# Kernel tuning notes

Measured on AMD Instinct MI355X. Metric: run time of the kernel, lower is better.

Reference implementation:

```python
import jax, jax.numpy as jnp
import numpy as np

T, S = 24, 200
N = T * S            # 4800 product-graph nodes
C_IN, C_W, C_OUT = 8, 32, 1
K = 3                # polynomial filter order
NB = 2               # number of GTCNN blocks


def setup_inputs() -> dict:
    key = jax.random.key(0)
    ks = jax.random.split(key, 12)
    At = jax.random.uniform(ks[0], (T, T), dtype=jnp.float32)
    At = (At + At.T) * 0.5  # symmetric, positive degrees
    As = jax.random.uniform(ks[1], (S, S), dtype=jnp.float32)
    As = (As + As.T) * 0.5
    return {
        "x_in": jax.random.normal(ks[2], (N, C_IN), dtype=jnp.float32),
        "Adj_t": At,
        "Adj_s": As,
        "H": jax.random.normal(ks[3], (NB, K, C_W, C_W), dtype=jnp.float32) * 0.1,
        "s": jax.random.normal(ks[4], (NB, 4), dtype=jnp.float32),
        "W_first": jax.random.normal(ks[5], (C_IN, C_W), dtype=jnp.float32) * 0.1,
        "b_first": jnp.zeros((C_W,), jnp.float32),
        "W_last": jax.random.normal(ks[6], (C_W, C_OUT), dtype=jnp.float32) * 0.1,
        "b_last": jnp.zeros((C_OUT,), jnp.float32),
        "mlp_W1": jax.random.normal(ks[7], (NB, C_IN + C_W, C_W), dtype=jnp.float32) * 0.1,
        "mlp_b1": jnp.zeros((NB, C_W), jnp.float32),
        "mlp_W2": jax.random.normal(ks[8], (NB, C_W, C_W), dtype=jnp.float32) * 0.1,
        "mlp_b2": jnp.zeros((NB, C_W), jnp.float32),
    }


def _sym_norm(A):
    # D^{-1/2} A D^{-1/2} / 2 as in GTCNN_v2.__init__
    dinv = 1.0 / jnp.sqrt(jnp.sum(A, axis=1))
    return (A * dinv[:, None] * dinv[None, :]) * 0.5


def reference(x_in, Adj_t, Adj_s, H, s, W_first, b_first, W_last, b_last,
              mlp_W1, mlp_b1, mlp_W2, mlp_b2):
    At = _sym_norm(Adj_t)
    As = _sym_norm(Adj_s)
    I_t = jnp.eye(T, dtype=At.dtype)
    I_s = jnp.eye(S, dtype=As.dtype)
    I_N = jnp.eye(N, dtype=At.dtype)

    x = x_in @ W_first + b_first  # [N, C_W]
    for b in range(NB):
        sb = s[b]
        # product-graph adjacency: s0*I + s1*(I_t (x) As) + s2*(At (x) I_s) + s3*(At (x) As)
        Adj = (sb[0] * I_N
               + sb[1] * jnp.kron(I_t, As)
               + sb[2] * jnp.kron(At, I_s)
               + sb[3] * jnp.kron(At, As))
        # sum_k A^k x H_k via the recurrence p_{k} = A p_{k-1} (same math as matrix_power)
        p = x
        acc = p @ H[b, 0]
        for k in range(1, K):
            p = Adj @ p
            acc = acc + p @ H[b, k]
        xt = jnp.tanh(acc)
        feat = jnp.concatenate([xt, x_in], axis=-1)  # [N, C_W + C_in]
        h = jax.nn.relu(feat @ mlp_W1[b] + mlp_b1[b])
        x = h @ mlp_W2[b] + mlp_b2[b]
    return x @ W_last + b_last  # [N, C_out]
```

## Files before the change

### kernel.cpp

```cpp
#include <hip/hip_runtime.h>
#include <math.h>

#define TT 24
#define SS 200
#define CIN 8
#define CW 32
#define NSC 6400
#define NTOT 153600

#define DSOFF   0
#define ATOFF   256
#define AT2OFF  832
#define XOFF    1408
#define M0AOFF  155008
#define M0BOFF  308608
#define M1OFF   462208
#define M2OFF   615808
#define M3OFF   769408

template<bool FIRST>
__global__ __launch_bounds__(1024)
void kSp(const float* __restrict__ xin, const float* __restrict__ At,
         const float* __restrict__ As, const float* __restrict__ Wf,
         const float* __restrict__ bf, const float* __restrict__ svec,
         float* __restrict__ ws, int b)
{
    __shared__ float4 sXd[SS];
    __shared__ float4 sX[SS];
    __shared__ float4 sU[SS];
    __shared__ float4 spart[4][SS];
    __shared__ float  sd[256];
    __shared__ float  sdt[TT];
    __shared__ float  sAt[TT*TT];

    const int tid = threadIdx.x;

    if (FIRST && blockIdx.x == 192) {
        if (tid < TT) {
            float sum = 0.f;
            #pragma unroll
            for (int i = 0; i < TT; ++i) sum += At[i*TT + tid];
            sdt[tid] = 1.f / sqrtf(sum);
        }
        __syncthreads();
        if (tid < TT*TT) {
            const int i = tid / TT, j = tid % TT;
            const float v = At[tid] * sdt[i] * sdt[j] * 0.5f;
            sAt[tid] = v;
            ws[ATOFF + tid] = v;
        }
        __syncthreads();
        if (tid < TT*TT) {
            const int i = tid / TT, j = tid % TT;
            float acc = 0.f;
            #pragma unroll
            for (int k = 0; k < TT; ++k) acc += sAt[i*TT + k] * sAt[k*TT + j];
            ws[AT2OFF + tid] = acc;
        }
        return;
    }

    const int q = tid >> 8;
    const int s = tid & 255;
    const bool act = s < SS;
    const int t  = blockIdx.x >> 3;
    const int c0 = (blockIdx.x & 7) * 4;

    if (FIRST) {
        if (act) {
            float v = 0.f;
            #pragma unroll 5
            for (int i = q*50; i < q*50 + 50; ++i) v += As[i*SS + s];
            spart[q][s].x = v;
        }
        __syncthreads();
        if (q == 0 && act) {
            const float sum = spart[0][s].x + spart[1][s].x
                            + spart[2][s].x + spart[3][s].x;
            const float d = 1.f / sqrtf(sum);
            sd[s] = d;
            if (blockIdx.x == 0) ws[DSOFF + s] = d;
        }
        __syncthreads();
    } else {
        if (tid < SS) sd[tid] = ws[DSOFF + tid];
        __syncthreads();
    }

    if (q == 0 && act) {
        float4 xv;
        if (FIRST) {
            const float4* xr = (const float4*)(xin + (t*SS + s)*CIN);
            const float4 xa = xr[0], xb = xr[1];
            float a0 = bf[c0], a1 = bf[c0+1], a2 = bf[c0+2], a3 = bf[c0+3];
            const float xi[8] = {xa.x, xa.y, xa.z, xa.w, xb.x, xb.y, xb.z, xb.w};
            #pragma unroll
            for (int i = 0; i < CIN; ++i) {
                a0 += xi[i] * Wf[i*CW + c0];
                a1 += xi[i] * Wf[i*CW + c0+1];
                a2 += xi[i] * Wf[i*CW + c0+2];
                a3 += xi[i] * Wf[i*CW + c0+3];
            }
            xv = make_float4(a0, a1, a2, a3);
            *(float4*)(ws + XOFF + t*NSC + s*CW + c0) = xv;
        } else {
            xv = *(const float4*)(ws + XOFF + t*NSC + s*CW + c0);
        }
        sX[s] = xv;
        const float d = sd[s];
        sXd[s] = make_float4(xv.x*d, xv.y*d, xv.z*d, xv.w*d);
    }
    __syncthreads();

    if (act) {
        float4 acc = make_float4(0.f, 0.f, 0.f, 0.f);
        #pragma unroll 5
        for (int sp = q*50; sp < q*50 + 50; ++sp) {
            const float a = As[sp*SS + s];
            const float4 xd = sXd[sp];
            acc.x += a*xd.x; acc.y += a*xd.y; acc.z += a*xd.z; acc.w += a*xd.w;
        }
        spart[q][s] = acc;
    }
    __syncthreads();
    float4 u1 = make_float4(0.f, 0.f, 0.f, 0.f);
    if (q == 0 && act) {
        const float4 p0 = spart[0][s], p1 = spart[1][s];
        const float4 p2 = spart[2][s], p3 = spart[3][s];
        const float h = 0.5f * sd[s];
        u1 = make_float4((p0.x+p1.x+p2.x+p3.x)*h, (p0.y+p1.y+p2.y+p3.y)*h,
                         (p0.z+p1.z+p2.z+p3.z)*h, (p0.w+p1.w+p2.w+p3.w)*h);
        const float d = sd[s];
        sU[s] = make_float4(u1.x*d, u1.y*d, u1.z*d, u1.w*d);
    }
    __syncthreads();

    if (act) {
        float4 acc = make_float4(0.f, 0.f, 0.f, 0.f);
        #pragma unroll 5
        for (int sp = q*50; sp < q*50 + 50; ++sp) {
            const float a = As[sp*SS + s];
            const float4 ud = sU[sp];
            acc.x += a*ud.x; acc.y += a*ud.y; acc.z += a*ud.z; acc.w += a*ud.w;
        }
        spart[q][s] = acc;
    }
    __syncthreads();
    if (q == 0 && act) {
        const float4 p0 = spart[0][s], p1 = spart[1][s];
        const float4 p2 = spart[2][s], p3 = spart[3][s];
        const float h = 0.5f * sd[s];
        const float4 u2 = make_float4((p0.x+p1.x+p2.x+p3.x)*h, (p0.y+p1.y+p2.y+p3.y)*h,
                                      (p0.z+p1.z+p2.z+p3.z)*h, (p0.w+p1.w+p2.w+p3.w)*h);
        const float s0 = svec[b*4+0], s1 = svec[b*4+1];
        const float s2 = svec[b*4+2], s3 = svec[b*4+3];
        const float b00 = s0*s0, b01 = 2.f*s0*s1, b02 = s1*s1;
        const float b10 = 2.f*s0*s2, b11 = 2.f*(s0*s3 + s1*s2), b12 = 2.f*s1*s3;
        const float b20 = s2*s2, b21 = 2.f*s2*s3, b22 = s3*s3;
        const float4 xv = sX[s];
        const int gid = t*NSC + s*CW + c0;
        *(float4*)(ws + M0AOFF + gid) = make_float4(
            s0*xv.x + s1*u1.x, s0*xv.y + s1*u1.y,
            s0*xv.z + s1*u1.z, s0*xv.w + s1*u1.w);
        *(float4*)(ws + M0BOFF + gid) = make_float4(
            b00*xv.x + b01*u1.x + b02*u2.x, b00*xv.y + b01*u1.y + b02*u2.y,
            b00*xv.z + b01*u1.z + b02*u2.z, b00*xv.w + b01*u1.w + b02*u2.w);
        *(float4*)(ws + M1OFF + gid) = make_float4(
            s2*xv.x + s3*u1.x, s2*xv.y + s3*u1.y,
            s2*xv.z + s3*u1.z, s2*xv.w + s3*u1.w);
        *(float4*)(ws + M2OFF + gid) = make_float4(
            b10*xv.x + b11*u1.x + b12*u2.x, b10*xv.y + b11*u1.y + b12*u2.y,
            b10*xv.z + b11*u1.z + b12*u2.z, b10*xv.w + b11*u1.w + b12*u2.w);
        *(float4*)(ws + M3OFF + gid) = make_float4(
            b20*xv.x + b21*u1.x + b22*u2.x, b20*xv.y + b21*u1.y + b22*u2.y,
            b20*xv.z + b21*u1.z + b22*u2.z, b20*xv.w + b21*u1.w + b22*u2.w);
    }
}

__global__ __launch_bounds__(256)
void kB(const float* __restrict__ xin, const float* __restrict__ H,
        const float* __restrict__ mW1, const float* __restrict__ mb1,
        const float* __restrict__ mW2, const float* __restrict__ mb2,
        const float* __restrict__ Wl, const float* __restrict__ bl,
        float* __restrict__ ws, float* __restrict__ out, int b, int last) {
    __shared__ float sAt[2*TT*TT];
    __shared__ float sH[3*CW*CW];
    __shared__ float sW1[(CW+CIN)*CW];
    __shared__ float sW2[CW*CW];
    __shared__ float sb1[CW], sb2[CW];
    __shared__ float sx[256], sp1[256], sp2[256], sxt[256], sh[256];
    __shared__ float sxin[8*CIN];

    const int tid = threadIdx.x;
    const int gid = blockIdx.x*256 + tid;
    const int t = gid / NSC;
    const int sc = gid - t*NSC;
    const int r = tid >> 5, c = tid & 31;
    const int node = gid >> 5;

    const float* Hb = H   + b*3*CW*CW;
    const float* W1 = mW1 + b*(CW+CIN)*CW;
    const float* W2 = mW2 + b*CW*CW;

    for (int i = tid; i < 2*TT*TT; i += 256) sAt[i] = ws[ATOFF + i];
    for (int i = tid; i < 3*CW*CW; i += 256) sH[i] = Hb[i];
    for (int i = tid; i < (CW+CIN)*CW; i += 256) sW1[i] = W1[i];
    for (int i = tid; i < CW*CW; i += 256) sW2[i] = W2[i];
    if (tid < CW) { sb1[tid] = mb1[b*CW + tid]; sb2[tid] = mb2[b*CW + tid]; }
    sx[tid] = ws[XOFF + gid];
    if (c < CIN) sxin[r*CIN + c] = xin[node*CIN + c];
    __syncthreads();

    {
        const float* M1 = ws + M1OFF + sc;
        const float* M2 = ws + M2OFF + sc;
        const float* M3 = ws + M3OFF + sc;
        float d1 = 0.f, d2 = 0.f, d3 = 0.f;
        #pragma unroll
        for (int tp = 0; tp < TT; ++tp) {
            const float a1 = sAt[t*TT + tp];
            const float a2 = sAt[TT*TT + t*TT + tp];
            d1 += a1 * M1[tp*NSC];
            d2 += a1 * M2[tp*NSC];
            d3 += a2 * M3[tp*NSC];
        }
        sp1[tid] = ws[M0AOFF + gid] + d1;
        sp2[tid] = ws[M0BOFF + gid] + d2 + d3;
    }
    __syncthreads();
    {
        float acc = 0.f;
        #pragma unroll 8
        for (int cp = 0; cp < CW; ++cp) {
            acc += sx[r*CW + cp]  * sH[cp*CW + c];
            acc += sp1[r*CW + cp] * sH[CW*CW + cp*CW + c];
            acc += sp2[r*CW + cp] * sH[2*CW*CW + cp*CW + c];
        }
        sxt[tid] = tanhf(acc);
    }
    __syncthreads();
    {
        float h = sb1[c];
        #pragma unroll 8
        for (int cp = 0; cp < CW; ++cp) h += sxt[r*CW + cp] * sW1[cp*CW + c];
        #pragma unroll
        for (int i = 0; i < CIN; ++i) h += sxin[r*CIN + i] * sW1[(CW+i)*CW + c];
        sh[tid] = fmaxf(h, 0.f);
    }
    __syncthreads();
    {
        float xn = sb2[c];
        #pragma unroll 8
        for (int cp = 0; cp < CW; ++cp) xn += sh[r*CW + cp] * sW2[cp*CW + c];
        if (!last) {
            ws[XOFF + gid] = xn;
        } else {
            float v = xn * Wl[c];
            #pragma unroll
            for (int off = 16; off; off >>= 1) v += __shfl_xor(v, off, 64);
            if (c == 0) out[node] = v + bl[0];
        }
    }
}

extern "C" void kernel_launch(void* const* d_in, const int* in_sizes, int n_in,
                              void* d_out, int out_size, void* d_ws, size_t ws_size,
                              hipStream_t stream) {
    const float* xin   = (const float*)d_in[0];
    const float* Adj_t = (const float*)d_in[1];
    const float* Adj_s = (const float*)d_in[2];
    const float* H     = (const float*)d_in[3];
    const float* svec  = (const float*)d_in[4];
    const float* Wf    = (const float*)d_in[5];
    const float* bf    = (const float*)d_in[6];
    const float* Wl    = (const float*)d_in[7];
    const float* bl    = (const float*)d_in[8];
    const float* mW1   = (const float*)d_in[9];
    const float* mb1   = (const float*)d_in[10];
    const float* mW2   = (const float*)d_in[11];
    const float* mb2   = (const float*)d_in[12];
    float* out = (float*)d_out;
    float* ws  = (float*)d_ws;

    kSp<true><<<193, 1024, 0, stream>>>(xin, Adj_t, Adj_s, Wf, bf, svec, ws, 0);
    kB<<<600, 256, 0, stream>>>(xin, H, mW1, mb1, mW2, mb2, Wl, bl,
                                ws, out, 0, 0);
    kSp<false><<<192, 1024, 0, stream>>>(xin, Adj_t, Adj_s, Wf, bf, svec, ws, 1);
    kB<<<600, 256, 0, stream>>>(xin, H, mW1, mb1, mW2, mb2, Wl, bl,
                                ws, out, 1, 1);
}
```

Measured before the change: 53.22 us.

## Fuse block-0 temporal mix and MLP with block-1 spatial filter into one kernel

Replaces the middle kB+kSp pair with a single kMid kernel of 96 blocks, each owning one time slice. Each block computes the temporal aggregation, tensor filter, tanh and MLP for all 200 nodes, keeps the resulting features in shared memory, and then runs block-1's spatial As products for an 8-channel slice. The point is to cut one launch and the global round-trip of X between stages. The cost is that each of the 4 blocks per time slice recomputes the full MLP for its slice. It also uses large shared memory at only 96 blocks, and the first kernel now has every 1024-thread block recompute the full As degree sums with only 200 active threads.

Measured after the change: 122.6 us. 130% more time.

```diff
diff --git a/kernel.cpp b/kernel.cpp
--- a/kernel.cpp
+++ b/kernel.cpp
@@ -8,34 +8,33 @@
 #define NSC 6400
 #define NTOT 153600
 
-#define DSOFF   0
-#define ATOFF   256
-#define AT2OFF  832
-#define XOFF    1408
-#define M0AOFF  155008
-#define M0BOFF  308608
-#define M1OFF   462208
-#define M2OFF   615808
-#define M3OFF   769408
-
-template<bool FIRST>
+#define DSOFF  0
+#define ATOFF  256
+#define AT2OFF 832
+#define XOFF   1408
+#define X1OFF  (XOFF  + NTOT)
+#define M0A0   (X1OFF + NTOT)
+#define M0B0   (M0A0 + NTOT)
+#define M10    (M0B0 + NTOT)
+#define M20    (M10  + NTOT)
+#define M30    (M20  + NTOT)
+#define M0A1   (M30  + NTOT)
+#define M0B1   (M0A1 + NTOT)
+#define M11    (M0B1 + NTOT)
+#define M21    (M11  + NTOT)
+#define M31    (M21  + NTOT)
+
 __global__ __launch_bounds__(1024)
-void kSp(const float* __restrict__ xin, const float* __restrict__ At,
-         const float* __restrict__ As, const float* __restrict__ Wf,
-         const float* __restrict__ bf, const float* __restrict__ svec,
-         float* __restrict__ ws, int b)
+void kSp0(const float* __restrict__ xin, const float* __restrict__ At,
+          const float* __restrict__ As, const float* __restrict__ Wf,
+          const float* __restrict__ bf, const float* __restrict__ svec,
+          float* __restrict__ ws)
 {
-    __shared__ float4 sXd[SS];
-    __shared__ float4 sX[SS];
-    __shared__ float4 sU[SS];
-    __shared__ float4 spart[4][SS];
-    __shared__ float  sd[256];
-    __shared__ float  sdt[TT];
-    __shared__ float  sAt[TT*TT];
-
+    __shared__ float4 sXd[SS], sXn[SS], sU[SS], spart[4][SS];
+    __shared__ float  sd[256], sdt[TT], sAt[TT*TT];
     const int tid = threadIdx.x;
 
-    if (FIRST && blockIdx.x == 192) {
+    if (blockIdx.x == 192) {
         if (tid < TT) {
             float sum = 0.f;
             #pragma unroll
@@ -66,82 +65,62 @@
     const int t  = blockIdx.x >> 3;
     const int c0 = (blockIdx.x & 7) * 4;
 
-    if (FIRST) {
-        if (act) {
-            float v = 0.f;
-            #pragma unroll 5
-            for (int i = q*50; i < q*50 + 50; ++i) v += As[i*SS + s];
-            spart[q][s].x = v;
-        }
-        __syncthreads();
-        if (q == 0 && act) {
-            const float sum = spart[0][s].x + spart[1][s].x
-                            + spart[2][s].x + spart[3][s].x;
-            const float d = 1.f / sqrtf(sum);
-            sd[s] = d;
-            if (blockIdx.x == 0) ws[DSOFF + s] = d;
-        }
-        __syncthreads();
-    } else {
-        if (tid < SS) sd[tid] = ws[DSOFF + tid];
-        __syncthreads();
-    }
-
-    if (q == 0 && act) {
-        float4 xv;
-        if (FIRST) {
-            const float4* xr = (const float4*)(xin + (t*SS + s)*CIN);
-            const float4 xa = xr[0], xb = xr[1];
-            float a0 = bf[c0], a1 = bf[c0+1], a2 = bf[c0+2], a3 = bf[c0+3];
-            const float xi[8] = {xa.x, xa.y, xa.z, xa.w, xb.x, xb.y, xb.z, xb.w};
-            #pragma unroll
-            for (int i = 0; i < CIN; ++i) {
-                a0 += xi[i] * Wf[i*CW + c0];
-                a1 += xi[i] * Wf[i*CW + c0+1];
-                a2 += xi[i] * Wf[i*CW + c0+2];
-                a3 += xi[i] * Wf[i*CW + c0+3];
-            }
-            xv = make_float4(a0, a1, a2, a3);
-            *(float4*)(ws + XOFF + t*NSC + s*CW + c0) = xv;
-        } else {
-            xv = *(const float4*)(ws + XOFF + t*NSC + s*CW + c0);
-        }
-        sX[s] = xv;
-        const float d = sd[s];
-        sXd[s] = make_float4(xv.x*d, xv.y*d, xv.z*d, xv.w*d);
-    }
-    __syncthreads();
-
+    if (tid < SS) {
+        float sum = 0.f;
+        #pragma unroll 8
+        for (int i = 0; i < SS; ++i) sum += As[i*SS + tid];
+        const float d = 1.f / sqrtf(sum);
+        sd[tid] = d;
+        if (blockIdx.x == 0) ws[DSOFF + tid] = d;
+    }
+    __syncthreads();
+
+    if (tid < SS) {
+        const float4 xa = *(const float4*)(xin + (t*SS + tid)*CIN);
+        const float4 xb = *(const float4*)(xin + (t*SS + tid)*CIN + 4);
+        const float xi[8] = {xa.x,xa.y,xa.z,xa.w,xb.x,xb.y,xb.z,xb.w};
+        float4 xv = *(const float4*)(bf + c0);
+        #pragma unroll
+        for (int i = 0; i < CIN; ++i) {
+            const float4 w = *(const float4*)(Wf + i*CW + c0);
+            xv.x += xi[i]*w.x; xv.y += xi[i]*w.y;
+            xv.z += xi[i]*w.z; xv.w += xi[i]*w.w;
+        }
+        *(float4*)(ws + XOFF + t*NSC + tid*CW + c0) = xv;
+        sXn[tid] = xv;
+        const float d = sd[tid];
+        sXd[tid] = make_float4(xv.x*d, xv.y*d, xv.z*d, xv.w*d);
+    }
+    __syncthreads();
+
+    float4 u1 = make_float4(0.f,0.f,0.f,0.f);
     if (act) {
-        float4 acc = make_float4(0.f, 0.f, 0.f, 0.f);
+        float4 acc = make_float4(0.f,0.f,0.f,0.f);
         #pragma unroll 5
         for (int sp = q*50; sp < q*50 + 50; ++sp) {
             const float a = As[sp*SS + s];
-            const float4 xd = sXd[sp];
-            acc.x += a*xd.x; acc.y += a*xd.y; acc.z += a*xd.z; acc.w += a*xd.w;
+            const float4 x = sXd[sp];
+            acc.x += a*x.x; acc.y += a*x.y; acc.z += a*x.z; acc.w += a*x.w;
         }
         spart[q][s] = acc;
     }
     __syncthreads();
-    float4 u1 = make_float4(0.f, 0.f, 0.f, 0.f);
     if (q == 0 && act) {
         const float4 p0 = spart[0][s], p1 = spart[1][s];
         const float4 p2 = spart[2][s], p3 = spart[3][s];
-        const float h = 0.5f * sd[s];
+        const float h = 0.5f * sd[s], d = sd[s];
         u1 = make_float4((p0.x+p1.x+p2.x+p3.x)*h, (p0.y+p1.y+p2.y+p3.y)*h,
                          (p0.z+p1.z+p2.z+p3.z)*h, (p0.w+p1.w+p2.w+p3.w)*h);
-        const float d = sd[s];
         sU[s] = make_float4(u1.x*d, u1.y*d, u1.z*d, u1.w*d);
     }
     __syncthreads();
-
     if (act) {
-        float4 acc = make_float4(0.f, 0.f, 0.f, 0.f);
+        float4 acc = make_float4(0.f,0.f,0.f,0.f);
         #pragma unroll 5
         for (int sp = q*50; sp < q*50 + 50; ++sp) {
             const float a = As[sp*SS + s];
-            const float4 ud = sU[sp];
-            acc.x += a*ud.x; acc.y += a*ud.y; acc.z += a*ud.z; acc.w += a*ud.w;
+            const float4 u = sU[sp];
+            acc.x += a*u.x; acc.y += a*u.y; acc.z += a*u.z; acc.w += a*u.w;
         }
         spart[q][s] = acc;
     }
@@ -152,37 +131,206 @@
         const float h = 0.5f * sd[s];
         const float4 u2 = make_float4((p0.x+p1.x+p2.x+p3.x)*h, (p0.y+p1.y+p2.y+p3.y)*h,
                                       (p0.z+p1.z+p2.z+p3.z)*h, (p0.w+p1.w+p2.w+p3.w)*h);
-        const float s0 = svec[b*4+0], s1 = svec[b*4+1];
-        const float s2 = svec[b*4+2], s3 = svec[b*4+3];
+        const float s0 = svec[0], s1 = svec[1], s2 = svec[2], s3 = svec[3];
         const float b00 = s0*s0, b01 = 2.f*s0*s1, b02 = s1*s1;
         const float b10 = 2.f*s0*s2, b11 = 2.f*(s0*s3 + s1*s2), b12 = 2.f*s1*s3;
         const float b20 = s2*s2, b21 = 2.f*s2*s3, b22 = s3*s3;
-        const float4 xv = sX[s];
-        const int gid = t*NSC + s*CW + c0;
-        *(float4*)(ws + M0AOFF + gid) = make_float4(
+        const float4 xv = sXn[s];
+        const int g4 = t*NSC + s*CW + c0;
+        *(float4*)(ws + M0A0 + g4) = make_float4(
             s0*xv.x + s1*u1.x, s0*xv.y + s1*u1.y,
             s0*xv.z + s1*u1.z, s0*xv.w + s1*u1.w);
-        *(float4*)(ws + M0BOFF + gid) = make_float4(
+        *(float4*)(ws + M0B0 + g4) = make_float4(
             b00*xv.x + b01*u1.x + b02*u2.x, b00*xv.y + b01*u1.y + b02*u2.y,
             b00*xv.z + b01*u1.z + b02*u2.z, b00*xv.w + b01*u1.w + b02*u2.w);
-        *(float4*)(ws + M1OFF + gid) = make_float4(
+        *(float4*)(ws + M10 + g4) = make_float4(
             s2*xv.x + s3*u1.x, s2*xv.y + s3*u1.y,
             s2*xv.z + s3*u1.z, s2*xv.w + s3*u1.w);
-        *(float4*)(ws + M2OFF + gid) = make_float4(
+        *(float4*)(ws + M20 + g4) = make_float4(
             b10*xv.x + b11*u1.x + b12*u2.x, b10*xv.y + b11*u1.y + b12*u2.y,
             b10*xv.z + b11*u1.z + b12*u2.z, b10*xv.w + b11*u1.w + b12*u2.w);
-        *(float4*)(ws + M3OFF + gid) = make_float4(
+        *(float4*)(ws + M30 + g4) = make_float4(
             b20*xv.x + b21*u1.x + b22*u2.x, b20*xv.y + b21*u1.y + b22*u2.y,
             b20*xv.z + b21*u1.z + b22*u2.z, b20*xv.w + b21*u1.w + b22*u2.w);
     }
 }
 
+__global__ __launch_bounds__(1024, 1)
+void kMid(const float* __restrict__ xin, const float* __restrict__ As,
+          const float* __restrict__ H, const float* __restrict__ svec,
+          const float* __restrict__ mW1, const float* __restrict__ mb1,
+          const float* __restrict__ mW2, const float* __restrict__ mb2,
+          float* __restrict__ ws)
+{
+    __shared__ float  sAtr[TT], sAt2r[TT];
+    __shared__ float  sH[3*CW*CW], sW1[(CW+CIN)*CW], sW2[CW*CW];
+    __shared__ float  sb1[CW], sb2[CW];
+    __shared__ float  sd[256];
+    __shared__ float  sx[NSC], sp1[NSC], sp2[NSC];
+    __shared__ float  sxt_l[1024], sh_l[1024];
+    __shared__ float  sxin[32*CIN];
+    __shared__ float4 sXd[SS], sU[SS], spart[4][SS];
+
+    const int tid  = threadIdx.x;
+    const int t    = blockIdx.x >> 2;
+    const int part = blockIdx.x & 3;
+
+    for (int i = tid; i < 3*CW*CW; i += 1024) sH[i] = H[i];
+    for (int i = tid; i < (CW+CIN)*CW; i += 1024) sW1[i] = mW1[i];
+    for (int i = tid; i < CW*CW; i += 1024) sW2[i] = mW2[i];
+    if (tid < CW) { sb1[tid] = mb1[tid]; sb2[tid] = mb2[tid]; }
+    if (tid < TT) { sAtr[tid] = ws[ATOFF + t*TT + tid];
+                    sAt2r[tid] = ws[AT2OFF + t*TT + tid]; }
+    if (tid < SS) sd[tid] = ws[DSOFF + tid];
+    __syncthreads();
+
+    for (int i = tid; i < NSC/4; i += 1024) {
+        float4 d1 = make_float4(0,0,0,0), d2 = d1, d3 = d1;
+        #pragma unroll
+        for (int tp = 0; tp < TT; ++tp) {
+            const float a1 = sAtr[tp], a2 = sAt2r[tp];
+            const float4 m1 = *((const float4*)(ws + M10) + tp*(NSC/4) + i);
+            const float4 m2 = *((const float4*)(ws + M20) + tp*(NSC/4) + i);
+            const float4 m3 = *((const float4*)(ws + M30) + tp*(NSC/4) + i);
+            d1.x += a1*m1.x; d1.y += a1*m1.y; d1.z += a1*m1.z; d1.w += a1*m1.w;
+            d2.x += a1*m2.x; d2.y += a1*m2.y; d2.z += a1*m2.z; d2.w += a1*m2.w;
+            d3.x += a2*m3.x; d3.y += a2*m3.y; d3.z += a2*m3.z; d3.w += a2*m3.w;
+        }
+        const float4 m0a = *((const float4*)(ws + M0A0) + t*(NSC/4) + i);
+        const float4 m0b = *((const float4*)(ws + M0B0) + t*(NSC/4) + i);
+        const float4 xv  = *((const float4*)(ws + XOFF) + t*(NSC/4) + i);
+        *(float4*)(sp1 + 4*i) = make_float4(m0a.x+d1.x, m0a.y+d1.y, m0a.z+d1.z, m0a.w+d1.w);
+        *(float4*)(sp2 + 4*i) = make_float4(m0b.x+d2.x+d3.x, m0b.y+d2.y+d3.y,
+                                            m0b.z+d2.z+d3.z, m0b.w+d2.w+d3.w);
+        *(float4*)(sx + 4*i) = xv;
+    }
+    __syncthreads();
+
+    for (int k = 0; k < 7; ++k) {
+        const int nl = tid >> 5, c = tid & 31;
+        const int node = k*32 + nl;
+        const bool on = node < SS;
+        if (on && c < CIN) sxin[nl*CIN + c] = xin[(t*SS + node)*CIN + c];
+        __syncthreads();
+        float xt = 0.f;
+        if (on) {
+            float acc = 0.f;
+            #pragma unroll 8
+            for (int cp = 0; cp < CW; ++cp) {
+                acc += sx[node*CW + cp]  * sH[cp*CW + c];
+                acc += sp1[node*CW + cp] * sH[CW*CW + cp*CW + c];
+                acc += sp2[node*CW + cp] * sH[2*CW*CW + cp*CW + c];
+            }
+            xt = tanhf(acc);
+        }
+        sxt_l[tid] = xt;
+        __syncthreads();
+        float hv = 0.f;
+        if (on) {
+            float h = sb1[c];
+            #pragma unroll 8
+            for (int cp = 0; cp < CW; ++cp) h += sxt_l[nl*CW + cp] * sW1[cp*CW + c];
+            #pragma unroll
+            for (int i = 0; i < CIN; ++i) h += sxin[nl*CIN + i] * sW1[(CW+i)*CW + c];
+            hv = fmaxf(h, 0.f);
+        }
+        sh_l[tid] = hv;
+        __syncthreads();
+        float xn = 0.f;
+        if (on) {
+            xn = sb2[c];
+            #pragma unroll 8
+            for (int cp = 0; cp < CW; ++cp) xn += sh_l[nl*CW + cp] * sW2[cp*CW + c];
+        }
+        __syncthreads();
+        if (on) {
+            sp1[node*CW + c] = xn;
+            if (part == 0) ws[X1OFF + t*NSC + node*CW + c] = xn;
+        }
+        __syncthreads();
+    }
+
+    const int q = tid >> 8, s = tid & 255;
+    const bool act = s < SS;
+    const float s0 = svec[4], s1 = svec[5], s2 = svec[6], s3 = svec[7];
+    const float b00 = s0*s0, b01 = 2.f*s0*s1, b02 = s1*s1;
+    const float b10 = 2.f*s0*s2, b11 = 2.f*(s0*s3 + s1*s2), b12 = 2.f*s1*s3;
+    const float b20 = s2*s2, b21 = 2.f*s2*s3, b22 = s3*s3;
+
+    for (int g = 0; g < 2; ++g) {
+        const int c0 = part*8 + g*4;
+        if (q == 0 && act) {
+            const float4 xv = *(const float4*)(sp1 + s*CW + c0);
+            const float d = sd[s];
+            sXd[s] = make_float4(xv.x*d, xv.y*d, xv.z*d, xv.w*d);
+        }
+        __syncthreads();
+        float4 u1 = make_float4(0.f,0.f,0.f,0.f);
+        if (act) {
+            float4 acc = make_float4(0.f,0.f,0.f,0.f);
+            #pragma unroll 5
+            for (int sp = q*50; sp < q*50 + 50; ++sp) {
+                const float a = As[sp*SS + s];
+                const float4 x = sXd[sp];
+                acc.x += a*x.x; acc.y += a*x.y; acc.z += a*x.z; acc.w += a*x.w;
+            }
+            spart[q][s] = acc;
+        }
+        __syncthreads();
+        if (q == 0 && act) {
+            const float4 p0 = spart[0][s], p1 = spart[1][s];
+            const float4 p2 = spart[2][s], p3 = spart[3][s];
+            const float h = 0.5f * sd[s], d = sd[s];
+            u1 = make_float4((p0.x+p1.x+p2.x+p3.x)*h, (p0.y+p1.y+p2.y+p3.y)*h,
+                             (p0.z+p1.z+p2.z+p3.z)*h, (p0.w+p1.w+p2.w+p3.w)*h);
+            sU[s] = make_float4(u1.x*d, u1.y*d, u1.z*d, u1.w*d);
+        }
+        __syncthreads();
+        if (act) {
+            float4 acc = make_float4(0.f,0.f,0.f,0.f);
+            #pragma unroll 5
+            for (int sp = q*50; sp < q*50 + 50; ++sp) {
+                const float a = As[sp*SS + s];
+                const float4 u = sU[sp];
+                acc.x += a*u.x; acc.y += a*u.y; acc.z += a*u.z; acc.w += a*u.w;
+            }
+            spart[q][s] = acc;
+        }
+        __syncthreads();
+        if (q == 0 && act) {
+            const float4 p0 = spart[0][s], p1 = spart[1][s];
+            const float4 p2 = spart[2][s], p3 = spart[3][s];
+            const float h = 0.5f * sd[s];
+            const float4 u2 = make_float4((p0.x+p1.x+p2.x+p3.x)*h, (p0.y+p1.y+p2.y+p3.y)*h,
+                                          (p0.z+p1.z+p2.z+p3.z)*h, (p0.w+p1.w+p2.w+p3.w)*h);
+            const float4 xv = *(const float4*)(sp1 + s*CW + c0);
+            const int g4 = t*NSC + s*CW + c0;
+            *(float4*)(ws + M0A1 + g4) = make_float4(
+                s0*xv.x + s1*u1.x, s0*xv.y + s1*u1.y,
+                s0*xv.z + s1*u1.z, s0*xv.w + s1*u1.w);
+            *(float4*)(ws + M0B1 + g4) = make_float4(
+                b00*xv.x + b01*u1.x + b02*u2.x, b00*xv.y + b01*u1.y + b02*u2.y,
+                b00*xv.z + b01*u1.z + b02*u2.z, b00*xv.w + b01*u1.w + b02*u2.w);
+            *(float4*)(ws + M11 + g4) = make_float4(
+                s2*xv.x + s3*u1.x, s2*xv.y + s3*u1.y,
+                s2*xv.z + s3*u1.z, s2*xv.w + s3*u1.w);
+            *(float4*)(ws + M21 + g4) = make_float4(
+                b10*xv.x + b11*u1.x + b12*u2.x, b10*xv.y + b11*u1.y + b12*u2.y,
+                b10*xv.z + b11*u1.z + b12*u2.z, b10*xv.w + b11*u1.w + b12*u2.w);
+            *(float4*)(ws + M31 + g4) = make_float4(
+                b20*xv.x + b21*u1.x + b22*u2.x, b20*xv.y + b21*u1.y + b22*u2.y,
+                b20*xv.z + b21*u1.z + b22*u2.z, b20*xv.w + b21*u1.w + b22*u2.w);
+        }
+        __syncthreads();
+    }
+}
+
 __global__ __launch_bounds__(256)
-void kB(const float* __restrict__ xin, const float* __restrict__ H,
-        const float* __restrict__ mW1, const float* __restrict__ mb1,
-        const float* __restrict__ mW2, const float* __restrict__ mb2,
-        const float* __restrict__ Wl, const float* __restrict__ bl,
-        float* __restrict__ ws, float* __restrict__ out, int b, int last) {
+void kBlast(const float* __restrict__ xin, const float* __restrict__ H,
+            const float* __restrict__ mW1, const float* __restrict__ mb1,
+            const float* __restrict__ mW2, const float* __restrict__ mb2,
+            const float* __restrict__ Wl, const float* __restrict__ bl,
+            float* __restrict__ ws, float* __restrict__ out) {
     __shared__ float sAt[2*TT*TT];
     __shared__ float sH[3*CW*CW];
     __shared__ float sW1[(CW+CIN)*CW];
@@ -198,23 +346,19 @@
     const int r = tid >> 5, c = tid & 31;
     const int node = gid >> 5;
 
-    const float* Hb = H   + b*3*CW*CW;
-    const float* W1 = mW1 + b*(CW+CIN)*CW;
-    const float* W2 = mW2 + b*CW*CW;
-
     for (int i = tid; i < 2*TT*TT; i += 256) sAt[i] = ws[ATOFF + i];
-    for (int i = tid; i < 3*CW*CW; i += 256) sH[i] = Hb[i];
-    for (int i = tid; i < (CW+CIN)*CW; i += 256) sW1[i] = W1[i];
-    for (int i = tid; i < CW*CW; i += 256) sW2[i] = W2[i];
-    if (tid < CW) { sb1[tid] = mb1[b*CW + tid]; sb2[tid] = mb2[b*CW + tid]; }
-    sx[tid] = ws[XOFF + gid];
+    for (int i = tid; i < 3*CW*CW; i += 256) sH[i] = H[3*CW*CW + i];
+    for (int i = tid; i < (CW+CIN)*CW; i += 256) sW1[i] = mW1[(CW+CIN)*CW + i];
+    for (int i = tid; i < CW*CW; i += 256) sW2[i] = mW2[CW*CW + i];
+    if (tid < CW) { sb1[tid] = mb1[CW + tid]; sb2[tid] = mb2[CW + tid]; }
+    sx[tid] = ws[X1OFF + gid];
     if (c < CIN) sxin[r*CIN + c] = xin[node*CIN + c];
     __syncthreads();
 
     {
-        const float* M1 = ws + M1OFF + sc;
-        const float* M2 = ws + M2OFF + sc;
-        const float* M3 = ws + M3OFF + sc;
+        const float* M1 = ws + M11 + sc;
+        const float* M2 = ws + M21 + sc;
+        const float* M3 = ws + M31 + sc;
         float d1 = 0.f, d2 = 0.f, d3 = 0.f;
         #pragma unroll
         for (int tp = 0; tp < TT; ++tp) {
@@ -224,8 +368,8 @@
             d2 += a1 * M2[tp*NSC];
             d3 += a2 * M3[tp*NSC];
         }
-        sp1[tid] = ws[M0AOFF + gid] + d1;
-        sp2[tid] = ws[M0BOFF + gid] + d2 + d3;
+        sp1[tid] = ws[M0A1 + gid] + d1;
+        sp2[tid] = ws[M0B1 + gid] + d2 + d3;
     }
     __syncthreads();
     {
@@ -252,14 +396,10 @@
         float xn = sb2[c];
         #pragma unroll 8
         for (int cp = 0; cp < CW; ++cp) xn += sh[r*CW + cp] * sW2[cp*CW + c];
-        if (!last) {
-            ws[XOFF + gid] = xn;
-        } else {
-            float v = xn * Wl[c];
-            #pragma unroll
-            for (int off = 16; off; off >>= 1) v += __shfl_xor(v, off, 64);
-            if (c == 0) out[node] = v + bl[0];
-        }
+        float v = xn * Wl[c];
+        #pragma unroll
+        for (int off = 16; off; off >>= 1) v += __shfl_xor(v, off, 64);
+        if (c == 0) out[node] = v + bl[0];
     }
 }
 
@@ -282,10 +422,7 @@
     float* out = (float*)d_out;
     float* ws  = (float*)d_ws;
 
-    kSp<true><<<193, 1024, 0, stream>>>(xin, Adj_t, Adj_s, Wf, bf, svec, ws, 0);
-    kB<<<600, 256, 0, stream>>>(xin, H, mW1, mb1, mW2, mb2, Wl, bl,
-                                ws, out, 0, 0);
-    kSp<false><<<192, 1024, 0, stream>>>(xin, Adj_t, Adj_s, Wf, bf, svec, ws, 1);
-    kB<<<600, 256, 0, stream>>>(xin, H, mW1, mb1, mW2, mb2, Wl, bl,
-                                ws, out, 1, 1);
+    kSp0<<<193, 1024, 0, stream>>>(xin, Adj_t, Adj_s, Wf, bf, svec, ws);
+    kMid<<<96, 1024, 0, stream>>>(xin, Adj_s, H, svec, mW1, mb1, mW2, mb2, ws);
+    kBlast<<<600, 256, 0, stream>>>(xin, H, mW1, mb1, mW2, mb2, Wl, bl, ws, out);
 }
```
